# Kernel tuning notes

Hardware: AMD Instinct MI355X
Metric: run time of the kernel (lower is better)

Reference implementation:

```python
import jax, jax.numpy as jnp
import numpy as np

B, C, H, W = 8, 384, 32, 32
N = 4                      # d_state
DI = 2 * C                 # d_inner = ssm_ratio * dim
R = -(-C // 16)            # dt_rank = ceil(dim/16) = 24
K = 4                      # scan directions
HID = 4 * C                # mlp hidden


def layer_norm(x, g, b, eps=1e-5):
    mu = jnp.mean(x, -1, keepdims=True)
    var = jnp.mean((x - mu) ** 2, -1, keepdims=True)
    return (x - mu) * jax.lax.rsqrt(var + eps) * g + b


def setup_inputs() -> dict:
    key = jax.random.key(0)
    ks = jax.random.split(key, 20)
    s = lambda k, shape, sc=0.02: jax.random.normal(k, shape, jnp.float32) * sc
    inp = {
        "x": jax.random.normal(ks[0], (B, C, H, W), jnp.float32),
        "ln1_g": jnp.ones((C,), jnp.float32), "ln1_b": jnp.zeros((C,), jnp.float32),
        "in_proj_W": s(ks[1], (2 * DI, C)),
        "conv_W": s(ks[2], (DI, 1, 3, 3), 0.1), "conv_b": jnp.zeros((DI,), jnp.float32),
        "x_proj_W": s(ks[3], (K, R + 2 * N, DI)),
        "dt_W": s(ks[4], (K, DI, R), 0.1), "dt_b": s(ks[5], (K, DI), 0.1),
        "A_log": jnp.log(jnp.tile(jnp.arange(1, N + 1, dtype=jnp.float32), (K, DI, 1))),
        "Ds": jnp.ones((K, DI), jnp.float32),
        "out_norm_g": jnp.ones((DI,), jnp.float32), "out_norm_b": jnp.zeros((DI,), jnp.float32),
        "out_proj_W": s(ks[6], (C, DI)),
        "ln2_g": jnp.ones((C,), jnp.float32), "ln2_b": jnp.zeros((C,), jnp.float32),
        "fc1_W": s(ks[7], (HID, C)), "fc1_b": jnp.zeros((HID,), jnp.float32),
        "fc2_W": s(ks[8], (C, HID)), "fc2_b": jnp.zeros((C,), jnp.float32),
    }
    return inp


def _block(x, ln1_g, ln1_b, in_proj_W, conv_W, conv_b, x_proj_W, dt_W, dt_b,
           A_log, Ds, out_norm_g, out_norm_b, out_proj_W, ln2_g, ln2_b,
           fc1_W, fc1_b, fc2_W, fc2_b):
    # x: (B,C,H,W) -> channels-last (B,H,W,C) as in mamba_fusion4
    xin = jnp.transpose(x, (0, 2, 3, 1))
    L = H * W
    shortcut = xin
    xn = layer_norm(xin, ln1_g, ln1_b)
    # ---- SS2D ----
    xz = jnp.einsum('bhwc,ec->bhwe', xn, in_proj_W)           # (B,H,W,2*DI)
    xs_, z = jnp.split(xz, 2, axis=-1)
    xc = jnp.transpose(xs_, (0, 3, 1, 2))                     # (B,DI,H,W)
    xc = jax.lax.conv_general_dilated(xc, conv_W, (1, 1), ((1, 1), (1, 1)),
                                      feature_group_count=DI)
    xc = jax.nn.silu(xc + conv_b[None, :, None, None])
    # cross-scan: 4 directions
    x_hw = xc.reshape(B, DI, L)
    x_wh = jnp.transpose(xc, (0, 1, 3, 2)).reshape(B, DI, L)
    xs = jnp.stack([x_hw, x_wh, jnp.flip(x_hw, -1), jnp.flip(x_wh, -1)], axis=1)  # (B,K,DI,L)
    x_dbl = jnp.einsum('bkdl,kcd->bkcl', xs, x_proj_W)
    dts, Bs, Cs = x_dbl[:, :, :R], x_dbl[:, :, R:R + N], x_dbl[:, :, R + N:]
    dts = jnp.einsum('bkrl,kdr->bkdl', dts, dt_W)
    dt = jax.nn.softplus(dts + dt_b[None, :, :, None])        # (B,K,DI,L)
    A = -jnp.exp(A_log)                                       # (K,DI,N)
    # selective scan, L-leading
    dt_l = jnp.transpose(dt, (3, 0, 1, 2))
    xs_l = jnp.transpose(xs, (3, 0, 1, 2))
    Bs_l = jnp.transpose(Bs, (3, 0, 1, 2))
    Cs_l = jnp.transpose(Cs, (3, 0, 1, 2))

    def step(h, inp):
        dtt, xt, Bt, Ct = inp                                  # (B,K,DI),(B,K,DI),(B,K,N),(B,K,N)
        h = jnp.exp(dtt[..., None] * A) * h + (dtt * xt)[..., None] * Bt[:, :, None, :]
        yt = jnp.einsum('bkdn,bkn->bkd', h, Ct)
        return h, yt

    h0 = jnp.zeros((B, K, DI, N), xs.dtype)
    _, ys = jax.lax.scan(step, h0, (dt_l, xs_l, Bs_l, Cs_l))   # ys: (L,B,K,DI)
    ys = jnp.transpose(ys, (1, 2, 3, 0))                       # (B,K,DI,L)
    ys = ys + xs * Ds[None, :, :, None]                        # skip D*u per direction
    # merge directions (invert flips / transposes)
    inv = jnp.flip(ys[:, 2:4], -1)
    wh = lambda t: jnp.transpose(t.reshape(B, DI, W, H), (0, 1, 3, 2)).reshape(B, DI, L)
    y = ys[:, 0] + inv[:, 0] + wh(ys[:, 1]) + wh(inv[:, 1])    # (B,DI,L)
    y = jnp.transpose(y, (0, 2, 1)).reshape(B, H, W, DI)
    y = layer_norm(y, out_norm_g, out_norm_b)
    y = y * jax.nn.silu(z)
    y = jnp.einsum('bhwd,cd->bhwc', y, out_proj_W)
    xr = shortcut + y
    # ---- MLP ----
    m = layer_norm(xr, ln2_g, ln2_b)
    m = jax.nn.gelu(jnp.einsum('bhwc,ec->bhwe', m, fc1_W) + fc1_b)
    m = jnp.einsum('bhwe,ce->bhwc', m, fc2_W) + fc2_b
    return xr + m                                              # (B,H,W,C)


def reference(x, ln1_g, ln1_b, in_proj_W, conv_W, conv_b, x_proj_W, dt_W, dt_b,
              A_log, Ds, out_norm_g, out_norm_b, out_proj_W, ln2_g, ln2_b,
              fc1_W, fc1_b, fc2_W, fc2_b):
    return _block(x, ln1_g, ln1_b, in_proj_W, conv_W, conv_b, x_proj_W, dt_W, dt_b,
                  A_log, Ds, out_norm_g, out_norm_b, out_proj_W, ln2_g, ln2_b,
                  fc1_W, fc1_b, fc2_W, fc2_b)
```

## Files before the change

### kernel.cpp

```cpp
#include <hip/hip_runtime.h>
#include <hip/hip_bf16.h>
#include <math.h>

#define LQ 1024
#define CC 384
#define DI 768
#define RR 24
#define NN 4
#define BB 8
#define NC 32
#define CL 32
#define LDP 40

typedef __attribute__((ext_vector_type(8))) short bf16x8;
typedef __attribute__((ext_vector_type(4))) float f32x4;

__device__ __forceinline__ float siluf(float v) { return v / (1.f + __expf(-v)); }
__device__ __forceinline__ float softplus_fast(float v) {
  float av = fabsf(v);
  float e = __expf(-av);
  return fmaxf(v, 0.f) + 0.69314718f * __log2f(1.f + e);
}
__device__ __forceinline__ float geluf(float x) {
  float u = 0.7978845608028654f * (x + 0.044715f * x * x * x);
  float e = __expf(2.f * u);
  float t = 1.f - 2.f / (e + 1.f);
  return 0.5f * x * (1.f + t);
}
__device__ __forceinline__ int trp(int l) { return ((l & 31) << 5) | (l >> 5); }
__device__ __forceinline__ short f2bf(float f) {
  union { float f; unsigned u; } v; v.f = f;
  unsigned r = (v.u + 0x7fffu + ((v.u >> 16) & 1u)) >> 16;
  return (short)r;
}
__device__ __forceinline__ float bf2f(unsigned short u) {
  union { unsigned u; float f; } v; v.u = ((unsigned)u) << 16; return v.f;
}
__device__ __forceinline__ bf16x8 pack8(float4 u, float4 v) {
  bf16x8 r;
  r[0] = f2bf(u.x); r[1] = f2bf(u.y); r[2] = f2bf(u.z); r[3] = f2bf(u.w);
  r[4] = f2bf(v.x); r[5] = f2bf(v.y); r[6] = f2bf(v.z); r[7] = f2bf(v.w);
  return r;
}
__device__ __forceinline__ void gload_lds16(const void* g, void* l) {
  __builtin_amdgcn_global_load_lds(
      (const __attribute__((address_space(1))) void*)g,
      (__attribute__((address_space(3))) void*)l, 16, 0, 0);
}
__device__ __forceinline__ void tile_barrier() {
  asm volatile("s_waitcnt lgkmcnt(0)" ::: "memory");
  __builtin_amdgcn_s_barrier();
  __builtin_amdgcn_sched_barrier(0);
}

__global__ __launch_bounds__(256) void wcvt_kernel(
    const float* __restrict__ w0, const float* __restrict__ w1,
    const float* __restrict__ w2, const float* __restrict__ w3,
    unsigned short* __restrict__ dst) {
  int gid = blockIdx.x * 256 + threadIdx.x;
  int e = gid * 8;
  const float* src; int off;
  if (e < 589824)        { src = w0; off = e; }
  else if (e < 884736)   { src = w1; off = e - 589824; }
  else if (e < 1474560)  { src = w2; off = e - 884736; }
  else                   { src = w3; off = e - 1474560; }
  float4 a = *(const float4*)(src + off);
  float4 b = *(const float4*)(src + off + 4);
  *(bf16x8*)(dst + e) = pack8(a, b);
}

__global__ __launch_bounds__(256) void ln1_transpose(
    const float* __restrict__ x, const float* __restrict__ g, const float* __restrict__ b,
    unsigned short* __restrict__ xn, unsigned short* __restrict__ xT) {
  __shared__ float xt[CC][65];
  __shared__ float reds[4][64], redq[4][64];
  __shared__ float mus[64], rvs[64];
  int blk = blockIdx.x;
  int bb = blk >> 4, l0 = (blk & 15) * 64;
  int tid = threadIdx.x;
  const float* xb = x + (size_t)bb * CC * LQ + l0;
#pragma unroll
  for (int it = 0; it < 96; ++it) {
    int idx = it * 256 + tid;
    int c = idx >> 6, i = idx & 63;
    xt[c][i] = xb[(size_t)c * LQ + i];
  }
  __syncthreads();
  int tok = tid & 63, cs = tid >> 6;
  float s = 0.f, sq = 0.f;
#pragma unroll 4
  for (int cc = 0; cc < 96; ++cc) {
    float v = xt[cs * 96 + cc][tok];
    s += v; sq += v * v;
  }
  reds[cs][tok] = s; redq[cs][tok] = sq;
  __syncthreads();
  if (tid < 64) {
    s = reds[0][tid] + reds[1][tid] + reds[2][tid] + reds[3][tid];
    sq = redq[0][tid] + redq[1][tid] + redq[2][tid] + redq[3][tid];
    float mu = s * (1.f / CC);
    float var = sq * (1.f / CC) - mu * mu;
    mus[tid] = mu; rvs[tid] = rsqrtf(var + 1e-5f);
  }
  __syncthreads();
  size_t obase = ((size_t)bb * LQ + l0) * CC;
#pragma unroll
  for (int it = 0; it < 96; ++it) {
    unsigned idx = it * 256 + tid;
    unsigned t = idx / CC, c = idx - t * CC;
    float v = xt[c][t];
    xT[obase + idx] = (unsigned short)f2bf(v);
    xn[obase + idx] = (unsigned short)f2bf((v - mus[t]) * rvs[t] * g[c] + b[c]);
  }
}

__global__ __launch_bounds__(64) void ln2_kernel(const float* __restrict__ in,
    const float* __restrict__ g, const float* __restrict__ b,
    unsigned short* __restrict__ out) {
  int t = blockIdx.x; int lane = threadIdx.x;
  float v[6]; float s = 0.f, sq = 0.f;
#pragma unroll
  for (int i = 0; i < 6; ++i) {
    int c = lane + i * 64;
    float x = in[(size_t)t * CC + c];
    v[i] = x; s += x; sq += x * x;
  }
#pragma unroll
  for (int off = 32; off > 0; off >>= 1) { s += __shfl_xor(s, off); sq += __shfl_xor(sq, off); }
  float mu = s * (1.f / CC);
  float var = sq * (1.f / CC) - mu * mu;
  float r = rsqrtf(var + 1e-5f);
#pragma unroll
  for (int i = 0; i < 6; ++i) {
    int c = lane + i * 64;
    out[(size_t)t * CC + c] = (unsigned short)f2bf((v[i] - mu) * r * g[c] + b[c]);
  }
}

template<int EPI, int BM>
__global__ __launch_bounds__(256, (BM == 128) ? 3 : 4) void gemm_lds(
    const unsigned short* __restrict__ A, const unsigned short* __restrict__ W,
    void* __restrict__ out0, void* __restrict__ out1,
    const float* __restrict__ bias, const void* __restrict__ add,
    int M, int N, int K) {
  constexpr int MF = BM / 32;
  __shared__ short smem[2 * BM * 32 + 2 * 128 * 32];
  const int tid = threadIdx.x;
  const int bm = blockIdx.x * BM, bn = blockIdx.y * 128;
  const int lane = tid & 63, w = tid >> 6;
  const int wm = (w >> 1) * (BM / 2), wn = (w & 1) * 64;
  const int l15 = lane & 15, l4 = lane >> 4;
  f32x4 acc[MF][4] = {};

  auto stage = [&](int t, int buf) {
    short* Ad = smem + buf * BM * 32;
    short* Wd = smem + 2 * BM * 32 + buf * 128 * 32;
#pragma unroll
    for (int q = 0; q < BM / 64; ++q) {
      int slot = q * 256 + tid;
      int row = slot >> 2, qtr = slot & 3;
      gload_lds16(A + (size_t)(bm + row) * K + t * 32 + qtr * 8,
                  Ad + (q * 256 + (tid & 192)) * 8);
    }
#pragma unroll
    for (int q = 0; q < 2; ++q) {
      int slot = q * 256 + tid;
      int row = slot >> 2, qtr = slot & 3;
      gload_lds16(W + (size_t)(bn + row) * K + t * 32 + qtr * 8,
                  Wd + (q * 256 + (tid & 192)) * 8);
    }
  };
  auto compute = [&](int buf) {
    const short* Ab = smem + buf * BM * 32;
    const short* Wb = smem + 2 * BM * 32 + buf * 128 * 32;
    bf16x8 af[MF], bf[4];
#pragma unroll
    for (int i = 0; i < MF; ++i)
      af[i] = *(const bf16x8*)&Ab[(wm + i * 16 + l15) * 32 + l4 * 8];
#pragma unroll
    for (int j = 0; j < 4; ++j)
      bf[j] = *(const bf16x8*)&Wb[(wn + j * 16 + l15) * 32 + l4 * 8];
#pragma unroll
    for (int i = 0; i < MF; ++i)
#pragma unroll
      for (int j = 0; j < 4; ++j)
        acc[i][j] = __builtin_amdgcn_mfma_f32_16x16x32_bf16(af[i], bf[j], acc[i][j], 0, 0, 0);
  };

  const int NT = K >> 5;
  stage(0, 0);
  __syncthreads();
  for (int t = 0; t < NT; ++t) {
    int cur = t & 1;
    if (t + 1 < NT) stage(t + 1, cur ^ 1);
    compute(cur);
    __syncthreads();
  }

  if constexpr (EPI == 0 || EPI == 2) {
    short* rep = smem;
    unsigned short* ob;
    int nb;
    if (EPI == 0) { ob = (bn < DI) ? (unsigned short*)out0 : (unsigned short*)out1; nb = bn % DI; }
    else          { ob = (unsigned short*)out0; nb = bn; }
    const int OD = (EPI == 0) ? DI : N;
#pragma unroll
    for (int p = 0; p < 2; ++p) {
      if (wm == p * 64) {
#pragma unroll
        for (int i = 0; i < 4; ++i) {
          int rrow = i * 16 + l4 * 4;
#pragma unroll
          for (int j = 0; j < 4; ++j) {
            int col = wn + j * 16 + l15;
            float bv = (EPI == 2) ? bias[bn + col] : 0.f;
#pragma unroll
            for (int q = 0; q < 4; ++q) {
              float val = acc[i][j][q] + bv;
              if (EPI == 2) val = geluf(val);
              rep[(rrow + q) * 136 + col] = f2bf(val);
            }
          }
        }
      }
      __syncthreads();
      int rrow = tid >> 2, rcg = (tid & 3) * 8;
#pragma unroll
      for (int it = 0; it < 4; ++it) {
        int col = rcg + it * 32;
        bf16x8 v = *(const bf16x8*)&rep[rrow * 136 + col];
        *(bf16x8*)&ob[(size_t)(bm + p * 64 + rrow) * OD + nb + col] = v;
      }
      __syncthreads();
    }
  } else {
    float* o = (float*)out0;
#pragma unroll
    for (int i = 0; i < MF; ++i) {
      int mb = bm + wm + i * 16 + l4 * 4;
#pragma unroll
      for (int j = 0; j < 4; ++j) {
        int n = bn + wn + j * 16 + l15;
#pragma unroll
        for (int q = 0; q < 4; ++q) {
          int m = mb + q;
          float val = acc[i][j][q];
          if (EPI == 1) {
            o[(size_t)m * CC + n] = val + bf2f(((const unsigned short*)add)[(size_t)m * CC + n]);
          } else {
            o[(size_t)m * CC + n] = val + bias[n] + ((const float*)add)[(size_t)m * CC + n];
          }
        }
      }
    }
  }
}

template<int EPI, int BN>
__global__ __launch_bounds__(256, 4) void gemm_mfma(
    const unsigned short* __restrict__ A, const float* __restrict__ W,
    void* __restrict__ out0, void* __restrict__ out1,
    const float* __restrict__ bias, const float* __restrict__ add,
    int M, int N, int K) {
  constexpr int NF = BN / 32;
  constexpr int WL = BN / 32;
  __shared__ short smem[2 * 64 * LDP + 2 * BN * LDP];
  short* As0 = smem;
  short* As1 = smem + 64 * LDP;
  short* Ws0 = smem + 2 * 64 * LDP;
  short* Ws1 = smem + 2 * 64 * LDP + BN * LDP;
  const int tid = threadIdx.x;
  const int bm = blockIdx.x * 64, bn = blockIdx.y * BN;
  const int lane = tid & 63, w = tid >> 6;
  const int wm = (w >> 1) * 32, wn = (w & 1) * (BN / 2);
  const int l15 = lane & 15, l4 = lane >> 4;
  f32x4 acc[2][NF] = {};
  const int ar = tid >> 2, ac = (tid & 3) * 8;
  const int wr = (BN == 128) ? (tid >> 1) : (tid >> 2);
  const int wc = (BN == 128) ? ((tid & 1) * 16) : ((tid & 3) * 8);
  const unsigned short* Agp = A + (size_t)(bm + ar) * K + ac;
  const float* Wgp = W + (size_t)(bn + wr) * K + wc;

  uint4 pa0, pa1;
  float4 pw0[WL], pw1[WL];

  auto loadT = [&](int t, uint4& pa, float4* pw) {
    pa = *(const uint4*)(Agp + t * 32);
#pragma unroll
    for (int i = 0; i < WL; ++i) pw[i] = *(const float4*)(Wgp + t * 32 + i * 4);
  };
  auto storeT = [&](short* Ad, short* Wd, const uint4& pa, const float4* pw) {
    *(uint4*)&Ad[ar * LDP + ac] = pa;
    short* wdst = &Wd[wr * LDP + wc];
#pragma unroll
    for (int i = 0; i < WL / 2; ++i)
      *(bf16x8*)(wdst + i * 8) = pack8(pw[2 * i], pw[2 * i + 1]);
  };
  auto computeT = [&](const short* Ab, const short* Wb) {
    bf16x8 af[2], bf[NF];
#pragma unroll
    for (int i = 0; i < 2; ++i)
      af[i] = *(const bf16x8*)&Ab[(wm + i * 16 + l15) * LDP + l4 * 8];
#pragma unroll
    for (int j = 0; j < NF; ++j)
      bf[j] = *(const bf16x8*)&Wb[(wn + j * 16 + l15) * LDP + l4 * 8];
#pragma unroll
    for (int i = 0; i < 2; ++i)
#pragma unroll
      for (int j = 0; j < NF; ++j)
        acc[i][j] = __builtin_amdgcn_mfma_f32_16x16x32_bf16(af[i], bf[j], acc[i][j], 0, 0, 0);
  };

  const int NT = K >> 5;
  loadT(0, pa0, pw0);
  storeT(As0, Ws0, pa0, pw0);
  loadT(1, pa1, pw1);
  tile_barrier();
  for (int t = 0; t < NT; t += 2) {
    if (t + 2 < NT) loadT(t + 2, pa0, pw0);
    computeT(As0, Ws0);
    storeT(As1, Ws1, pa1, pw1);
    tile_barrier();
    if (t + 3 < NT) loadT(t + 3, pa1, pw1);
    computeT(As1, Ws1);
    if (t + 2 < NT) storeT(As0, Ws0, pa0, pw0);
    tile_barrier();
  }
#pragma unroll
  for (int i = 0; i < 2; ++i) {
    int mb = bm + wm + i * 16 + l4 * 4;
#pragma unroll
    for (int j = 0; j < NF; ++j) {
      int n = bn + wn + j * 16 + l15;
#pragma unroll
      for (int q = 0; q < 4; ++q) {
        int m = mb + q;
        ((float*)out0)[(size_t)m * N + n] = acc[i][j][q];
      }
    }
  }
}

__global__ __launch_bounds__(256) void dt_gemm(
    const float* __restrict__ xdbl, const float* __restrict__ dtW,
    const float* __restrict__ dtb, unsigned short* __restrict__ dt_all) {
  __shared__ short smem[128 * 136];
  short* As = smem;
  short* Ws = smem + 128 * LDP;
  const int tid = threadIdx.x;
  const int bm = blockIdx.x * 128;
  const int kk = blockIdx.y / 6, nt = blockIdx.y % 6;
  const int n0 = nt * 128;
  const int lane = tid & 63, w = tid >> 6;
  const int wm = (w >> 1) * 64, wn = (w & 1) * 64;
  const int l15 = lane & 15, l4 = lane >> 4;
  const int r = tid >> 1, half = (tid & 1) * 16;
  {
    const float* Ag = xdbl + (size_t)(bm + r) * 128 + kk * 32 + half;
    float4 a0 = *(const float4*)(Ag);
    float4 a1 = *(const float4*)(Ag + 4);
    float4 a2 = *(const float4*)(Ag + 8);
    float4 a3 = *(const float4*)(Ag + 12);
    short* asw = &As[r * LDP + half];
    *(bf16x8*)asw = pack8(a0, a1);
    *(bf16x8*)(asw + 8) = pack8(a2, a3);
    const float* Wg = dtW + ((size_t)kk * DI + n0 + r) * RR;
    bf16x8 qa, qb;
    if (half == 0) {
      float4 w0 = *(const float4*)(Wg);
      float4 w1 = *(const float4*)(Wg + 4);
      float4 w2 = *(const float4*)(Wg + 8);
      float4 w3 = *(const float4*)(Wg + 12);
      qa = pack8(w0, w1);
      qb = pack8(w2, w3);
    } else {
      float4 w0 = *(const float4*)(Wg + 16);
      float4 w1 = *(const float4*)(Wg + 20);
      qa = pack8(w0, w1);
      qb[0] = 0; qb[1] = 0; qb[2] = 0; qb[3] = 0;
      qb[4] = 0; qb[5] = 0; qb[6] = 0; qb[7] = 0;
    }
    short* wsw = &Ws[r * LDP + half];
    *(bf16x8*)wsw = qa;
    *(bf16x8*)(wsw + 8) = qb;
  }
  __syncthreads();
  f32x4 acc[4][4] = {};
  {
    const short* ap = &As[(wm + l15) * LDP + l4 * 8];
    const short* bp = &Ws[(wn + l15) * LDP + l4 * 8];
    bf16x8 af[4], bf[4];
#pragma unroll
    for (int f = 0; f < 4; ++f) af[f] = *(const bf16x8*)(ap + f * 16 * LDP);
#pragma unroll
    for (int f = 0; f < 4; ++f) bf[f] = *(const bf16x8*)(bp + f * 16 * LDP);
#pragma unroll
    for (int i = 0; i < 4; ++i)
#pragma unroll
      for (int j = 0; j < 4; ++j)
        acc[i][j] = __builtin_amdgcn_mfma_f32_16x16x32_bf16(af[i], bf[j], acc[i][j], 0, 0, 0);
  }
  __syncthreads();
#pragma unroll
  for (int j = 0; j < 4; ++j) {
    int col = wn + j * 16 + l15;
    float bv = dtb[kk * DI + n0 + col];
#pragma unroll
    for (int i = 0; i < 4; ++i) {
      int mrow = wm + i * 16 + l4 * 4;
#pragma unroll
      for (int q = 0; q < 4; ++q)
        smem[(mrow + q) * 136 + col] = f2bf(softplus_fast(acc[i][j][q] + bv));
    }
  }
  __syncthreads();
  const int row0 = tid >> 4, cg = (tid & 15) * 8;
#pragma unroll
  for (int it = 0; it < 8; ++it) {
    int row = row0 + it * 16;
    bf16x8 v = *(const bf16x8*)&smem[row * 136 + cg];
    *(bf16x8*)&dt_all[(size_t)(bm + row) * 3072 + kk * DI + n0 + cg] = v;
  }
}

__global__ __launch_bounds__(256) void conv_silu_kernel(
    const unsigned short* __restrict__ xs_, const float* __restrict__ cw,
    const float* __restrict__ cb, unsigned short* __restrict__ xcT) {
  int idx = blockIdx.x * 256 + threadIdx.x;
  int dg = idx % 96;
  int rem = idx / 96;
  int hq = rem & 7;
  int w = (rem >> 3) & 31;
  int b = rem >> 8;
  int d0 = dg * 8;
  int h0 = hq * 4;
  float wbuf[72];
#pragma unroll
  for (int i = 0; i < 18; ++i)
    *(float4*)&wbuf[i * 4] = *(const float4*)(cw + d0 * 9 + i * 4);
  float bias[8];
  *(float4*)&bias[0] = *(const float4*)(cb + d0);
  *(float4*)&bias[4] = *(const float4*)(cb + d0 + 4);
  float acc[4][8];
#pragma unroll
  for (int i = 0; i < 4; ++i)
#pragma unroll
    for (int j = 0; j < 8; ++j) acc[i][j] = bias[j];
  const unsigned short* xb = xs_ + (size_t)b * LQ * DI + d0;
#pragma unroll
  for (int hh = -1; hh <= 4; ++hh) {
    int h = h0 + hh;
    if (h < 0 || h > 31) continue;
#pragma unroll
    for (int dw = -1; dw <= 1; ++dw) {
      int ww = w + dw;
      if (ww < 0 || ww > 31) continue;
      bf16x8 xv = *(const bf16x8*)&xb[(size_t)(h * 32 + ww) * DI];
      float xf[8];
#pragma unroll
      for (int j = 0; j < 8; ++j) xf[j] = bf2f((unsigned short)xv[j]);
#pragma unroll
      for (int i = 0; i < 4; ++i) {
        int dh = hh - i;
        if (dh < -1 || dh > 1) continue;
        int tap = (dh + 1) * 3 + (dw + 1);
#pragma unroll
        for (int j = 0; j < 8; ++j) acc[i][j] += xf[j] * wbuf[j * 9 + tap];
      }
    }
  }
  unsigned short* ob = xcT + (size_t)b * LQ * DI + d0;
#pragma unroll
  for (int i = 0; i < 4; ++i) {
    bf16x8 v;
#pragma unroll
    for (int j = 0; j < 8; ++j) v[j] = f2bf(siluf(acc[i][j]));
    *(bf16x8*)&ob[(size_t)((h0 + i) * 32 + w) * DI] = v;
  }
}

__global__ __launch_bounds__(256) void scan_pass1(
    const unsigned short* __restrict__ xcT, const float* __restrict__ xdbl,
    const unsigned short* __restrict__ dtq,
    const float* __restrict__ A_log, float* __restrict__ Hc, float* __restrict__ Pc) {
  __shared__ float xlB[CL][4];
  int c = blockIdx.x, dc = blockIdx.y, bk = blockIdx.z;
  int b = bk >> 2, k = bk & 3;
  int tid = threadIdx.x;
  int d = dc * 256 + tid;
  const int kg = k & 1;
  const bool fl = k >= 2;
  int pos0 = kg ? c : c * CL;
  int dpos = kg ? 32 : 1;
  if (fl) { pos0 = 1023 - pos0; dpos = -dpos; }
  if (tid < CL) {
    int pos = pos0 + tid * dpos;
    *(float4*)&xlB[tid][0] =
        *(const float4*)(xdbl + ((size_t)b * LQ + pos) * 128 + k * 32 + 24);
  }
  float4 al = *(const float4*)&A_log[((size_t)k * DI + d) * NN];
  float A[NN] = {-__expf(al.x), -__expf(al.y), -__expf(al.z), -__expf(al.w)};
  float h[NN] = {0.f, 0.f, 0.f, 0.f};
  float sdt = 0.f;
  const unsigned short* dtp = dtq + ((size_t)b * LQ + pos0) * 3072 + k * DI + d;
  const unsigned short* xcp = xcT + ((size_t)b * LQ + pos0) * DI + d;
  const ptrdiff_t sDT = (ptrdiff_t)dpos * 3072;
  const ptrdiff_t sXC = (ptrdiff_t)dpos * DI;
  float dv[2][4], xv[2][4];
#pragma unroll
  for (int u = 0; u < 4; ++u) {
    dv[0][u] = bf2f(dtp[(ptrdiff_t)u * sDT]);
    xv[0][u] = bf2f(xcp[(ptrdiff_t)u * sXC]);
  }
  __syncthreads();
#pragma unroll
  for (int gg = 0; gg < 8; ++gg) {
    const int cur = gg & 1, nxt = cur ^ 1;
    if (gg < 7) {
#pragma unroll
      for (int u = 0; u < 4; ++u) {
        int j = (gg + 1) * 4 + u;
        dv[nxt][u] = bf2f(dtp[(ptrdiff_t)j * sDT]);
        xv[nxt][u] = bf2f(xcp[(ptrdiff_t)j * sXC]);
      }
    }
#pragma unroll
    for (int u = 0; u < 4; ++u) {
      int j = gg * 4 + u;
      float dt = dv[cur][u], xval = xv[cur][u];
      float4 Bv = *(const float4*)&xlB[j][0];
      float dx = dt * xval;
      sdt += dt;
      float a;
      a = __expf(dt * A[0]); h[0] = a * h[0] + dx * Bv.x;
      a = __expf(dt * A[1]); h[1] = a * h[1] + dx * Bv.y;
      a = __expf(dt * A[2]); h[2] = a * h[2] + dx * Bv.z;
      a = __expf(dt * A[3]); h[3] = a * h[3] + dx * Bv.w;
    }
  }
  size_t base = (((size_t)bk * NC + c) * DI + d) * 4;
  *(float4*)&Hc[base] = make_float4(h[0], h[1], h[2], h[3]);
  *(float4*)&Pc[base] = make_float4(__expf(sdt * A[0]), __expf(sdt * A[1]),
                                    __expf(sdt * A[2]), __expf(sdt * A[3]));
}

__global__ __launch_bounds__(256) void scan_pass2(
    float* __restrict__ Hc, const float* __restrict__ Pc) {
  int idx = blockIdx.x * 256 + threadIdx.x;
  int bk = idx / DI, d = idx - bk * DI;
  size_t base0 = (((size_t)bk * NC) * DI + d) * 4;
  const size_t cstr = (size_t)DI * 4;
  float4 hin = make_float4(0.f, 0.f, 0.f, 0.f);
  float4 hl = *(const float4*)&Hc[base0];
  float4 p  = *(const float4*)&Pc[base0];
  for (int c = 0; c < NC; ++c) {
    float4 hl_n = hl, p_n = p;
    if (c + 1 < NC) {
      size_t bn = base0 + (size_t)(c + 1) * cstr;
      hl_n = *(const float4*)&Hc[bn];
      p_n  = *(const float4*)&Pc[bn];
    }
    *(float4*)&Hc[base0 + (size_t)c * cstr] = hin;
    hin.x = hl.x + p.x * hin.x;
    hin.y = hl.y + p.y * hin.y;
    hin.z = hl.z + p.z * hin.z;
    hin.w = hl.w + p.w * hin.w;
    hl = hl_n; p = p_n;
  }
}

__global__ __launch_bounds__(256) void scan_pass3(
    const unsigned short* __restrict__ xcT, const float* __restrict__ xdbl,
    const unsigned short* __restrict__ dtq,
    const float* __restrict__ A_log, const float* __restrict__ Ds,
    const float* __restrict__ Hin,
    unsigned short* __restrict__ ym1, unsigned short* __restrict__ ym2) {
  __shared__ unsigned short ylds[CL][256];
  __shared__ float xbca[CL][8], xbcb[CL][8];
  int c = blockIdx.x, dc = blockIdx.y, bg = blockIdx.z;
  int b = bg >> 1, g = bg & 1;
  int tid = threadIdx.x;
  int d = dc * 256 + tid;
  int ka = g, kb = g + 2;
  int ca = c, cb = NC - 1 - c;
  int pa0 = g ? ca : ca * CL;
  int dpa = g ? 32 : 1;
  int pb0 = g ? (1023 - cb) : (1023 - cb * CL);
  if (tid < CL) {
    int pos = pa0 + tid * dpa;
    const float* p = xdbl + ((size_t)b * LQ + pos) * 128 + ka * 32 + 24;
    *(float4*)&xbca[tid][0] = *(const float4*)p;
    *(float4*)&xbca[tid][4] = *(const float4*)(p + 4);
  } else if (tid < 2 * CL) {
    int t2 = tid - CL;
    int pos = pb0 - t2 * dpa;
    const float* p = xdbl + ((size_t)b * LQ + pos) * 128 + kb * 32 + 24;
    *(float4*)&xbcb[t2][0] = *(const float4*)p;
    *(float4*)&xbcb[t2][4] = *(const float4*)(p + 4);
  }
  float4 ala = *(const float4*)&A_log[((size_t)ka * DI + d) * NN];
  float4 alb = *(const float4*)&A_log[((size_t)kb * DI + d) * NN];
  float Aa[NN] = {-__expf(ala.x), -__expf(ala.y), -__expf(ala.z), -__expf(ala.w)};
  float Ab[NN] = {-__expf(alb.x), -__expf(alb.y), -__expf(alb.z), -__expf(alb.w)};
  float Da = Ds[ka * DI + d], Db = Ds[kb * DI + d];
  size_t basea = (((size_t)(b * 4 + ka) * NC + ca) * DI + d) * 4;
  size_t baseb = (((size_t)(b * 4 + kb) * NC + cb) * DI + d) * 4;
  float4 h4a = *(const float4*)&Hin[basea];
  float4 h4b = *(const float4*)&Hin[baseb];
  float ha[NN] = {h4a.x, h4a.y, h4a.z, h4a.w};
  float hb[NN] = {h4b.x, h4b.y, h4b.z, h4b.w};
  unsigned short* ym = g ? ym2 : ym1;
  const unsigned short* dta_p = dtq + ((size_t)b * LQ + pa0) * 3072 + ka * DI + d;
  const unsigned short* dtb_p = dtq + ((size_t)b * LQ + pb0) * 3072 + kb * DI + d;
  const unsigned short* xca_p = xcT + ((size_t)b * LQ + pa0) * DI + d;
  const unsigned short* xcb_p = xcT + ((size_t)b * LQ + pb0) * DI + d;
  const ptrdiff_t sDT = (ptrdiff_t)dpa * 3072;
  const ptrdiff_t sXC = (ptrdiff_t)dpa * DI;
  float dva[2][4], dvb[2][4], xva[2][4], xvb[2][4];
#pragma unroll
  for (int u = 0; u < 4; ++u) {
    dva[0][u] = bf2f(dta_p[(ptrdiff_t)u * sDT]);
    dvb[0][u] = bf2f(dtb_p[-(ptrdiff_t)u * sDT]);
    xva[0][u] = bf2f(xca_p[(ptrdiff_t)u * sXC]);
    xvb[0][u] = bf2f(xcb_p[-(ptrdiff_t)u * sXC]);
  }
  __syncthreads();
#pragma unroll
  for (int gg = 0; gg < 8; ++gg) {
    const int cur = gg & 1, nxt = cur ^ 1;
    if (gg < 7) {
#pragma unroll
      for (int u = 0; u < 4; ++u) {
        int j = (gg + 1) * 4 + u;
        dva[nxt][u] = bf2f(dta_p[(ptrdiff_t)j * sDT]);
        dvb[nxt][u] = bf2f(dtb_p[-(ptrdiff_t)j * sDT]);
        xva[nxt][u] = bf2f(xca_p[(ptrdiff_t)j * sXC]);
        xvb[nxt][u] = bf2f(xcb_p[-(ptrdiff_t)j * sXC]);
      }
    }
#pragma unroll
    for (int u = 0; u < 4; ++u) {
      int j = gg * 4 + u;
      float dta = dva[cur][u], dtb2 = dvb[cur][u];
      float xa = xva[cur][u], xb = xvb[cur][u];
      float4 Ba = *(const float4*)&xbca[j][0];
      float4 Ca = *(const float4*)&xbca[j][4];
      float4 Bb = *(const float4*)&xbcb[j][0];
      float4 Cb = *(const float4*)&xbcb[j][4];
      float dxa = dta * xa, dxb = dtb2 * xb;
      float ya = xa * Da, yb = xb * Db;
      float a;
      a = __expf(dta * Aa[0]); ha[0] = a * ha[0] + dxa * Ba.x; ya += ha[0] * Ca.x;
      a = __expf(dta * Aa[1]); ha[1] = a * ha[1] + dxa * Ba.y; ya += ha[1] * Ca.y;
      a = __expf(dta * Aa[2]); ha[2] = a * ha[2] + dxa * Ba.z; ya += ha[2] * Ca.z;
      a = __expf(dta * Aa[3]); ha[3] = a * ha[3] + dxa * Ba.w; ya += ha[3] * Ca.w;
      a = __expf(dtb2 * Ab[0]); hb[0] = a * hb[0] + dxb * Bb.x; yb += hb[0] * Cb.x;
      a = __expf(dtb2 * Ab[1]); hb[1] = a * hb[1] + dxb * Bb.y; yb += hb[1] * Cb.y;
      a = __expf(dtb2 * Ab[2]); hb[2] = a * hb[2] + dxb * Bb.z; yb += hb[2] * Cb.z;
      a = __expf(dtb2 * Ab[3]); hb[3] = a * hb[3] + dxb * Bb.w; yb += hb[3] * Cb.w;
      if (j < CL / 2) {
        ylds[j][tid] = (unsigned short)f2bf(ya);
        ylds[CL - 1 - j][tid] = (unsigned short)f2bf(yb);
      } else {
        ylds[j][tid] = (unsigned short)f2bf(bf2f(ylds[j][tid]) + ya);
        ylds[CL - 1 - j][tid] = (unsigned short)f2bf(bf2f(ylds[CL - 1 - j][tid]) + yb);
      }
    }
  }
  unsigned short* ymp = ym + ((size_t)b * LQ + pa0) * DI + d;
  for (int s = 0; s < CL; ++s) {
    *ymp = ylds[s][tid];
    ymp += sXC;
  }
}

__global__ __launch_bounds__(256) void outnorm_mult_kernel(
    const unsigned short* __restrict__ ym1, const unsigned short* __restrict__ ym2,
    const unsigned short* __restrict__ z, const float* __restrict__ g,
    const float* __restrict__ bta, unsigned short* __restrict__ out) {
  int t = blockIdx.x, tid = threadIdx.x;
  __shared__ float red[8];
  float v[3]; float s = 0.f, sq = 0.f;
#pragma unroll
  for (int i = 0; i < 3; ++i) {
    int dd = tid + i * 256;
    float y = bf2f(ym1[(size_t)t * DI + dd]) + bf2f(ym2[(size_t)t * DI + dd]);
    v[i] = y; s += y; sq += y * y;
  }
#pragma unroll
  for (int off = 32; off > 0; off >>= 1) { s += __shfl_xor(s, off); sq += __shfl_xor(sq, off); }
  int wid = tid >> 6;
  if ((tid & 63) == 0) { red[wid] = s; red[4 + wid] = sq; }
  __syncthreads();
  s = red[0] + red[1] + red[2] + red[3];
  sq = red[4] + red[5] + red[6] + red[7];
  float mu = s * (1.f / DI), var = sq * (1.f / DI) - mu * mu;
  float r = rsqrtf(var + 1e-5f);
#pragma unroll
  for (int i = 0; i < 3; ++i) {
    int dd = tid + i * 256;
    float zv = bf2f(z[(size_t)t * DI + dd]);
    out[(size_t)t * DI + dd] =
        (unsigned short)f2bf(((v[i] - mu) * r * g[dd] + bta[dd]) * siluf(zv));
  }
}

extern "C" void kernel_launch(void* const* d_in, const int* in_sizes, int n_in,
                              void* d_out, int out_size, void* d_ws, size_t ws_size,
                              hipStream_t stream) {
  const float* x          = (const float*)d_in[0];
  const float* ln1_g      = (const float*)d_in[1];
  const float* ln1_b      = (const float*)d_in[2];
  const float* in_proj_W  = (const float*)d_in[3];
  const float* conv_W     = (const float*)d_in[4];
  const float* conv_b     = (const float*)d_in[5];
  const float* x_proj_W   = (const float*)d_in[6];
  const float* dt_W       = (const float*)d_in[7];
  const float* dt_b       = (const float*)d_in[8];
  const float* A_log      = (const float*)d_in[9];
  const float* Ds         = (const float*)d_in[10];
  const float* out_norm_g = (const float*)d_in[11];
  const float* out_norm_b = (const float*)d_in[12];
  const float* out_proj_W = (const float*)d_in[13];
  const float* ln2_g      = (const float*)d_in[14];
  const float* ln2_b      = (const float*)d_in[15];
  const float* fc1_W      = (const float*)d_in[16];
  const float* fc1_b      = (const float*)d_in[17];
  const float* fc2_W      = (const float*)d_in[18];
  const float* fc2_b      = (const float*)d_in[19];

  const int M = BB * LQ;
  char* RA = (char*)d_ws;
  char* RB = RA + 12582912;
  char* RC = RB + 25165824;
  char* RD = RC + 12582912;
  char* RE = RD + 25165824;
  char* RF = RE + 12582912;
  char* RG = RF + 4194304;
  char* RH = RG + 50331648;

  unsigned short* xn  = (unsigned short*)RA;
  float*          Hc  = (float*)RA;
  float*          xr  = (float*)RA;
  unsigned short* xs_ = (unsigned short*)RB;
  float*          Pc  = (float*)RB;
  unsigned short* ym1 = (unsigned short*)RB;
  unsigned short* m1  = (unsigned short*)RB;
  unsigned short* z   = (unsigned short*)RC;
  unsigned short* m0  = (unsigned short*)RC;
  unsigned short* ym2 = (unsigned short*)RD;
  unsigned short* xcT = (unsigned short*)RE;
  unsigned short* mn  = (unsigned short*)RE;
  float*          xdbl = (float*)RF;
  unsigned short* dtq = (unsigned short*)RG;
  unsigned short* xT  = (unsigned short*)RH;
  unsigned short* wbf = (unsigned short*)(RH + 6291456);
  unsigned short* wb_inproj  = wbf;
  unsigned short* wb_outproj = wbf + 589824;
  unsigned short* wb_fc1     = wbf + 884736;
  unsigned short* wb_fc2     = wbf + 1474560;

  wcvt_kernel<<<1008, 256, 0, stream>>>(in_proj_W, out_proj_W, fc1_W, fc2_W, wbf);
  ln1_transpose<<<128, 256, 0, stream>>>(x, ln1_g, ln1_b, xn, xT);
  gemm_lds<0, 128><<<dim3(M / 128, 12), 256, 0, stream>>>(
      xn, wb_inproj, xs_, z, nullptr, nullptr, M, 1536, CC);
  conv_silu_kernel<<<768, 256, 0, stream>>>(xs_, conv_W, conv_b, xcT);
  gemm_mfma<4, 64><<<dim3(M / 64, 2), 256, 0, stream>>>(
      xcT, x_proj_W, xdbl, nullptr, nullptr, nullptr, M, 128, DI);
  dt_gemm<<<dim3(M / 128, 24), 256, 0, stream>>>(xdbl, dt_W, dt_b, dtq);
  scan_pass1<<<dim3(NC, 3, BB * 4), 256, 0, stream>>>(
      xcT, xdbl, dtq, A_log, Hc, Pc);
  scan_pass2<<<(BB * 4 * DI) / 256, 256, 0, stream>>>(Hc, Pc);
  scan_pass3<<<dim3(NC, 3, BB * 2), 256, 0, stream>>>(
      xcT, xdbl, dtq, A_log, Ds, Hc, ym1, ym2);
  outnorm_mult_kernel<<<M, 256, 0, stream>>>(ym1, ym2, z, out_norm_g, out_norm_b, mn);
  gemm_lds<1, 64><<<dim3(M / 64, 3), 256, 0, stream>>>(
      mn, wb_outproj, xr, nullptr, nullptr, xT, M, 384, DI);
  ln2_kernel<<<M, 64, 0, stream>>>(xr, ln2_g, ln2_b, m0);
  gemm_lds<2, 128><<<dim3(M / 128, 12), 256, 0, stream>>>(
      m0, wb_fc1, m1, nullptr, fc1_b, nullptr, M, 1536, CC);
  gemm_lds<3, 64><<<dim3(M / 64, 3), 256, 0, stream>>>(
      m1, wb_fc2, (float*)d_out, nullptr, fc2_b, xr, M, 384, 1536);
}
```

Measured before the change: 246.8 us.

## Stage scan inputs in LDS via direct loads and parallelize chunk-state scan with shuffles

scan_pass1 and scan_pass3 now bulk-load each chunk's dt and xc tiles into shared memory with direct global-to-LDS 16-byte loads before the recurrence. This replaces the per-thread strided 2-byte register-prefetched global loads. scan_pass3 also keeps outputs in a register array instead of bf16 LDS read-modify-write, which avoids double bf16 rounding. scan_pass2 replaces the serial 32-step carry loop per chain with a warp-shuffle parallel prefix scan over the chunks. The cost is much more LDS per block in pass3 (about 64KB, which limits occupancy), more registers for y[32], and one thread per chunk in pass2.

New measurement: 276.2 us. +11.9%, slower.

```diff
diff --git a/kernel.cpp b/kernel.cpp
--- a/kernel.cpp
+++ b/kernel.cpp
@@ -483,16 +483,32 @@
     const unsigned short* __restrict__ xcT, const float* __restrict__ xdbl,
     const unsigned short* __restrict__ dtq,
     const float* __restrict__ A_log, float* __restrict__ Hc, float* __restrict__ Pc) {
+  __shared__ unsigned short dtl[CL * 256];
+  __shared__ unsigned short xcl[CL * 256];
   __shared__ float xlB[CL][4];
   int c = blockIdx.x, dc = blockIdx.y, bk = blockIdx.z;
   int b = bk >> 2, k = bk & 3;
   int tid = threadIdx.x;
-  int d = dc * 256 + tid;
+  int d0 = dc * 256;
+  int d = d0 + tid;
   const int kg = k & 1;
   const bool fl = k >= 2;
   int pos0 = kg ? c : c * CL;
   int dpos = kg ? 32 : 1;
   if (fl) { pos0 = 1023 - pos0; dpos = -dpos; }
+  {
+    int r = tid >> 5;
+    int cb = (tid & 31) * 8;
+    int wbase = (tid & 192) * 16;
+#pragma unroll
+    for (int q = 0; q < 4; ++q) {
+      ptrdiff_t pos = pos0 + (ptrdiff_t)(q * 8 + r) * dpos;
+      gload_lds16(dtq + ((size_t)b * LQ + pos) * 3072 + k * DI + d0 + cb,
+                  (char*)dtl + q * 4096 + wbase);
+      gload_lds16(xcT + ((size_t)b * LQ + pos) * DI + d0 + cb,
+                  (char*)xcl + q * 4096 + wbase);
+    }
+  }
   if (tid < CL) {
     int pos = pos0 + tid * dpos;
     *(float4*)&xlB[tid][0] =
@@ -502,41 +518,19 @@
   float A[NN] = {-__expf(al.x), -__expf(al.y), -__expf(al.z), -__expf(al.w)};
   float h[NN] = {0.f, 0.f, 0.f, 0.f};
   float sdt = 0.f;
-  const unsigned short* dtp = dtq + ((size_t)b * LQ + pos0) * 3072 + k * DI + d;
-  const unsigned short* xcp = xcT + ((size_t)b * LQ + pos0) * DI + d;
-  const ptrdiff_t sDT = (ptrdiff_t)dpos * 3072;
-  const ptrdiff_t sXC = (ptrdiff_t)dpos * DI;
-  float dv[2][4], xv[2][4];
-#pragma unroll
-  for (int u = 0; u < 4; ++u) {
-    dv[0][u] = bf2f(dtp[(ptrdiff_t)u * sDT]);
-    xv[0][u] = bf2f(xcp[(ptrdiff_t)u * sXC]);
-  }
-  __syncthreads();
-#pragma unroll
-  for (int gg = 0; gg < 8; ++gg) {
-    const int cur = gg & 1, nxt = cur ^ 1;
-    if (gg < 7) {
-#pragma unroll
-      for (int u = 0; u < 4; ++u) {
-        int j = (gg + 1) * 4 + u;
-        dv[nxt][u] = bf2f(dtp[(ptrdiff_t)j * sDT]);
-        xv[nxt][u] = bf2f(xcp[(ptrdiff_t)j * sXC]);
-      }
-    }
-#pragma unroll
-    for (int u = 0; u < 4; ++u) {
-      int j = gg * 4 + u;
-      float dt = dv[cur][u], xval = xv[cur][u];
-      float4 Bv = *(const float4*)&xlB[j][0];
-      float dx = dt * xval;
-      sdt += dt;
-      float a;
-      a = __expf(dt * A[0]); h[0] = a * h[0] + dx * Bv.x;
-      a = __expf(dt * A[1]); h[1] = a * h[1] + dx * Bv.y;
-      a = __expf(dt * A[2]); h[2] = a * h[2] + dx * Bv.z;
-      a = __expf(dt * A[3]); h[3] = a * h[3] + dx * Bv.w;
-    }
+  __syncthreads();
+#pragma unroll
+  for (int j = 0; j < CL; ++j) {
+    float dt = bf2f(dtl[j * 256 + tid]);
+    float xv = bf2f(xcl[j * 256 + tid]);
+    float4 Bv = *(const float4*)&xlB[j][0];
+    float dx = dt * xv;
+    sdt += dt;
+    float a;
+    a = __expf(dt * A[0]); h[0] = a * h[0] + dx * Bv.x;
+    a = __expf(dt * A[1]); h[1] = a * h[1] + dx * Bv.y;
+    a = __expf(dt * A[2]); h[2] = a * h[2] + dx * Bv.z;
+    a = __expf(dt * A[3]); h[3] = a * h[3] + dx * Bv.w;
   }
   size_t base = (((size_t)bk * NC + c) * DI + d) * 4;
   *(float4*)&Hc[base] = make_float4(h[0], h[1], h[2], h[3]);
@@ -546,27 +540,29 @@
 
 __global__ __launch_bounds__(256) void scan_pass2(
     float* __restrict__ Hc, const float* __restrict__ Pc) {
-  int idx = blockIdx.x * 256 + threadIdx.x;
-  int bk = idx / DI, d = idx - bk * DI;
-  size_t base0 = (((size_t)bk * NC) * DI + d) * 4;
-  const size_t cstr = (size_t)DI * 4;
-  float4 hin = make_float4(0.f, 0.f, 0.f, 0.f);
-  float4 hl = *(const float4*)&Hc[base0];
-  float4 p  = *(const float4*)&Pc[base0];
-  for (int c = 0; c < NC; ++c) {
-    float4 hl_n = hl, p_n = p;
-    if (c + 1 < NC) {
-      size_t bn = base0 + (size_t)(c + 1) * cstr;
-      hl_n = *(const float4*)&Hc[bn];
-      p_n  = *(const float4*)&Pc[bn];
-    }
-    *(float4*)&Hc[base0 + (size_t)c * cstr] = hin;
-    hin.x = hl.x + p.x * hin.x;
-    hin.y = hl.y + p.y * hin.y;
-    hin.z = hl.z + p.z * hin.z;
-    hin.w = hl.w + p.w * hin.w;
-    hl = hl_n; p = p_n;
-  }
+  int t = blockIdx.x * 256 + threadIdx.x;
+  int c = t & 31;
+  int chain = t >> 5;
+  int bk = chain / DI, d = chain - bk * DI;
+  size_t base = (((size_t)bk * NC + c) * DI + d) * 4;
+  float4 h = *(const float4*)&Hc[base];
+  float4 p = *(const float4*)&Pc[base];
+#pragma unroll
+  for (int s = 1; s < NC; s <<= 1) {
+    float hx = __shfl_up(h.x, s, 32), hy = __shfl_up(h.y, s, 32);
+    float hz = __shfl_up(h.z, s, 32), hw = __shfl_up(h.w, s, 32);
+    float px = __shfl_up(p.x, s, 32), py = __shfl_up(p.y, s, 32);
+    float pz = __shfl_up(p.z, s, 32), pw = __shfl_up(p.w, s, 32);
+    if (c >= s) {
+      h.x += p.x * hx; h.y += p.y * hy; h.z += p.z * hz; h.w += p.w * hw;
+      p.x *= px; p.y *= py; p.z *= pz; p.w *= pw;
+    }
+  }
+  float4 he;
+  he.x = __shfl_up(h.x, 1, 32); he.y = __shfl_up(h.y, 1, 32);
+  he.z = __shfl_up(h.z, 1, 32); he.w = __shfl_up(h.w, 1, 32);
+  if (c == 0) { he.x = 0.f; he.y = 0.f; he.z = 0.f; he.w = 0.f; }
+  *(float4*)&Hc[base] = he;
 }
 
 __global__ __launch_bounds__(256) void scan_pass3(
@@ -575,17 +571,37 @@
     const float* __restrict__ A_log, const float* __restrict__ Ds,
     const float* __restrict__ Hin,
     unsigned short* __restrict__ ym1, unsigned short* __restrict__ ym2) {
-  __shared__ unsigned short ylds[CL][256];
+  __shared__ unsigned short dtla[CL * 256], xcla[CL * 256];
+  __shared__ unsigned short dtlb[CL * 256], xclb[CL * 256];
   __shared__ float xbca[CL][8], xbcb[CL][8];
   int c = blockIdx.x, dc = blockIdx.y, bg = blockIdx.z;
   int b = bg >> 1, g = bg & 1;
   int tid = threadIdx.x;
-  int d = dc * 256 + tid;
+  int d0 = dc * 256;
+  int d = d0 + tid;
   int ka = g, kb = g + 2;
   int ca = c, cb = NC - 1 - c;
   int pa0 = g ? ca : ca * CL;
   int dpa = g ? 32 : 1;
   int pb0 = g ? (1023 - cb) : (1023 - cb * CL);
+  {
+    int r = tid >> 5;
+    int cbo = (tid & 31) * 8;
+    int wbase = (tid & 192) * 16;
+#pragma unroll
+    for (int q = 0; q < 4; ++q) {
+      ptrdiff_t posa = pa0 + (ptrdiff_t)(q * 8 + r) * dpa;
+      ptrdiff_t posb = pb0 - (ptrdiff_t)(q * 8 + r) * dpa;
+      gload_lds16(dtq + ((size_t)b * LQ + posa) * 3072 + ka * DI + d0 + cbo,
+                  (char*)dtla + q * 4096 + wbase);
+      gload_lds16(xcT + ((size_t)b * LQ + posa) * DI + d0 + cbo,
+                  (char*)xcla + q * 4096 + wbase);
+      gload_lds16(dtq + ((size_t)b * LQ + posb) * 3072 + kb * DI + d0 + cbo,
+                  (char*)dtlb + q * 4096 + wbase);
+      gload_lds16(xcT + ((size_t)b * LQ + posb) * DI + d0 + cbo,
+                  (char*)xclb + q * 4096 + wbase);
+    }
+  }
   if (tid < CL) {
     int pos = pa0 + tid * dpa;
     const float* p = xdbl + ((size_t)b * LQ + pos) * 128 + ka * 32 + 24;
@@ -610,66 +626,40 @@
   float ha[NN] = {h4a.x, h4a.y, h4a.z, h4a.w};
   float hb[NN] = {h4b.x, h4b.y, h4b.z, h4b.w};
   unsigned short* ym = g ? ym2 : ym1;
-  const unsigned short* dta_p = dtq + ((size_t)b * LQ + pa0) * 3072 + ka * DI + d;
-  const unsigned short* dtb_p = dtq + ((size_t)b * LQ + pb0) * 3072 + kb * DI + d;
-  const unsigned short* xca_p = xcT + ((size_t)b * LQ + pa0) * DI + d;
-  const unsigned short* xcb_p = xcT + ((size_t)b * LQ + pb0) * DI + d;
-  const ptrdiff_t sDT = (ptrdiff_t)dpa * 3072;
+  float y[CL];
+  __syncthreads();
+#pragma unroll
+  for (int j = 0; j < CL; ++j) {
+    float dta = bf2f(dtla[j * 256 + tid]);
+    float dtb2 = bf2f(dtlb[j * 256 + tid]);
+    float xa = bf2f(xcla[j * 256 + tid]);
+    float xb = bf2f(xclb[j * 256 + tid]);
+    float4 Ba = *(const float4*)&xbca[j][0];
+    float4 Ca = *(const float4*)&xbca[j][4];
+    float4 Bb = *(const float4*)&xbcb[j][0];
+    float4 Cb = *(const float4*)&xbcb[j][4];
+    float dxa = dta * xa, dxb = dtb2 * xb;
+    float ya = xa * Da, yb = xb * Db;
+    float a;
+    a = __expf(dta * Aa[0]); ha[0] = a * ha[0] + dxa * Ba.x; ya += ha[0] * Ca.x;
+    a = __expf(dta * Aa[1]); ha[1] = a * ha[1] + dxa * Ba.y; ya += ha[1] * Ca.y;
+    a = __expf(dta * Aa[2]); ha[2] = a * ha[2] + dxa * Ba.z; ya += ha[2] * Ca.z;
+    a = __expf(dta * Aa[3]); ha[3] = a * ha[3] + dxa * Ba.w; ya += ha[3] * Ca.w;
+    a = __expf(dtb2 * Ab[0]); hb[0] = a * hb[0] + dxb * Bb.x; yb += hb[0] * Cb.x;
+    a = __expf(dtb2 * Ab[1]); hb[1] = a * hb[1] + dxb * Bb.y; yb += hb[1] * Cb.y;
+    a = __expf(dtb2 * Ab[2]); hb[2] = a * hb[2] + dxb * Bb.z; yb += hb[2] * Cb.z;
+    a = __expf(dtb2 * Ab[3]); hb[3] = a * hb[3] + dxb * Bb.w; yb += hb[3] * Cb.w;
+    if (j < CL / 2) {
+      y[j] = ya; y[CL - 1 - j] = yb;
+    } else {
+      y[j] += ya; y[CL - 1 - j] += yb;
+    }
+  }
+  unsigned short* ymp = ym + ((size_t)b * LQ + pa0) * DI + d;
   const ptrdiff_t sXC = (ptrdiff_t)dpa * DI;
-  float dva[2][4], dvb[2][4], xva[2][4], xvb[2][4];
-#pragma unroll
-  for (int u = 0; u < 4; ++u) {
-    dva[0][u] = bf2f(dta_p[(ptrdiff_t)u * sDT]);
-    dvb[0][u] = bf2f(dtb_p[-(ptrdiff_t)u * sDT]);
-    xva[0][u] = bf2f(xca_p[(ptrdiff_t)u * sXC]);
-    xvb[0][u] = bf2f(xcb_p[-(ptrdiff_t)u * sXC]);
-  }
-  __syncthreads();
-#pragma unroll
-  for (int gg = 0; gg < 8; ++gg) {
-    const int cur = gg & 1, nxt = cur ^ 1;
-    if (gg < 7) {
-#pragma unroll
-      for (int u = 0; u < 4; ++u) {
-        int j = (gg + 1) * 4 + u;
-        dva[nxt][u] = bf2f(dta_p[(ptrdiff_t)j * sDT]);
-        dvb[nxt][u] = bf2f(dtb_p[-(ptrdiff_t)j * sDT]);
-        xva[nxt][u] = bf2f(xca_p[(ptrdiff_t)j * sXC]);
-        xvb[nxt][u] = bf2f(xcb_p[-(ptrdiff_t)j * sXC]);
-      }
-    }
-#pragma unroll
-    for (int u = 0; u < 4; ++u) {
-      int j = gg * 4 + u;
-      float dta = dva[cur][u], dtb2 = dvb[cur][u];
-      float xa = xva[cur][u], xb = xvb[cur][u];
-      float4 Ba = *(const float4*)&xbca[j][0];
-      float4 Ca = *(const float4*)&xbca[j][4];
-      float4 Bb = *(const float4*)&xbcb[j][0];
-      float4 Cb = *(const float4*)&xbcb[j][4];
-      float dxa = dta * xa, dxb = dtb2 * xb;
-      float ya = xa * Da, yb = xb * Db;
-      float a;
-      a = __expf(dta * Aa[0]); ha[0] = a * ha[0] + dxa * Ba.x; ya += ha[0] * Ca.x;
-      a = __expf(dta * Aa[1]); ha[1] = a * ha[1] + dxa * Ba.y; ya += ha[1] * Ca.y;
-      a = __expf(dta * Aa[2]); ha[2] = a * ha[2] + dxa * Ba.z; ya += ha[2] * Ca.z;
-      a = __expf(dta * Aa[3]); ha[3] = a * ha[3] + dxa * Ba.w; ya += ha[3] * Ca.w;
-      a = __expf(dtb2 * Ab[0]); hb[0] = a * hb[0] + dxb * Bb.x; yb += hb[0] * Cb.x;
-      a = __expf(dtb2 * Ab[1]); hb[1] = a * hb[1] + dxb * Bb.y; yb += hb[1] * Cb.y;
-      a = __expf(dtb2 * Ab[2]); hb[2] = a * hb[2] + dxb * Bb.z; yb += hb[2] * Cb.z;
-      a = __expf(dtb2 * Ab[3]); hb[3] = a * hb[3] + dxb * Bb.w; yb += hb[3] * Cb.w;
-      if (j < CL / 2) {
-        ylds[j][tid] = (unsigned short)f2bf(ya);
-        ylds[CL - 1 - j][tid] = (unsigned short)f2bf(yb);
-      } else {
-        ylds[j][tid] = (unsigned short)f2bf(bf2f(ylds[j][tid]) + ya);
-        ylds[CL - 1 - j][tid] = (unsigned short)f2bf(bf2f(ylds[CL - 1 - j][tid]) + yb);
-      }
-    }
-  }
-  unsigned short* ymp = ym + ((size_t)b * LQ + pa0) * DI + d;
+#pragma unroll
   for (int s = 0; s < CL; ++s) {
-    *ymp = ylds[s][tid];
+    *ymp = (unsigned short)f2bf(y[s]);
     ymp += sXC;
   }
 }
@@ -770,7 +760,7 @@
   dt_gemm<<<dim3(M / 128, 24), 256, 0, stream>>>(xdbl, dt_W, dt_b, dtq);
   scan_pass1<<<dim3(NC, 3, BB * 4), 256, 0, stream>>>(
       xcT, xdbl, dtq, A_log, Hc, Pc);
-  scan_pass2<<<(BB * 4 * DI) / 256, 256, 0, stream>>>(Hc, Pc);
+  scan_pass2<<<3072, 256, 0, stream>>>(Hc, Pc);
   scan_pass3<<<dim3(NC, 3, BB * 2), 256, 0, stream>>>(
       xcT, xdbl, dtq, A_log, Ds, Hc, ym1, ym2);
   outnorm_mult_kernel<<<M, 256, 0, stream>>>(ym1, ym2, z, out_norm_g, out_norm_b, mn);
```
